# Kernel tuning notes

Measured on AMD Instinct MI355X. Metric: run time of the kernel, lower is better.

## Reference

```python
import jax, jax.numpy as jnp
import numpy as np

EMBED_DIM = 128
B, SQ, SKV = 16, 2048, 2048


def setup_inputs() -> dict:
    key = jax.random.key(0)
    ks = jax.random.split(key, 8)
    d = EMBED_DIM
    scale = 1.0 / np.sqrt(d)
    return {
        "x": jax.random.normal(ks[0], (B, SQ, d), dtype=jnp.float32),
        "y": jax.random.normal(ks[1], (B, SKV, d), dtype=jnp.float32),
        "Wq": jax.random.normal(ks[2], (d, d), dtype=jnp.float32) * scale,
        "bq": jax.random.normal(ks[3], (d,), dtype=jnp.float32) * 0.02,
        "Wk": jax.random.normal(ks[4], (d, d), dtype=jnp.float32) * scale,
        "bk": jax.random.normal(ks[5], (d,), dtype=jnp.float32) * 0.02,
        "Wv": jax.random.normal(ks[6], (d, d), dtype=jnp.float32) * scale,
        "bv": jax.random.normal(ks[7], (d,), dtype=jnp.float32) * 0.02,
    }


def reference(x, y, Wq, bq, Wk, bk, Wv, bv):
    # Linear projections (torch Linear: x @ W.T + b; here W stored as [in,out])
    q = x @ Wq + bq            # [B, SQ, d]
    k = y @ Wk + bk            # [B, SKV, d]
    v = y @ Wv + bv            # [B, SKV, d]
    # Source scales by q.size(-1)**0.5 = sqrt(embed_dim)
    inv_scale = 1.0 / jnp.sqrt(jnp.asarray(q.shape[-1], q.dtype))
    scores = jnp.einsum("bqd,bkd->bqk", q, k) * inv_scale  # [B, SQ, SKV]
    attn = jax.nn.softmax(scores, axis=-1)
    return jnp.einsum("bqk,bkd->bqd", attn, v)
```

## Files before the change

kernel.cpp:

```cpp
#include <hip/hip_runtime.h>
#include <hip/hip_bf16.h>

typedef unsigned short ushort_t;
typedef __attribute__((ext_vector_type(8))) short short8;
typedef __attribute__((ext_vector_type(4))) float f32x4;
typedef __attribute__((ext_vector_type(16))) float f32x16;

#define MFMA16(a, b, c) __builtin_amdgcn_mfma_f32_16x16x32_bf16((a), (b), (c), 0, 0, 0)
#define MFMA32(a, b, c) __builtin_amdgcn_mfma_f32_32x32x16_bf16((a), (b), (c), 0, 0, 0)

__device__ __forceinline__ ushort_t f2bf(float f) {
    return __builtin_bit_cast(ushort_t, __float2bfloat16(f));
}

#define CVTPK(lo, hi) ({ unsigned int r_; \
    asm("v_cvt_pk_bf16_f32 %0, %1, %2" : "=v"(r_) : "v"(lo), "v"(hi)); r_; })

__device__ __forceinline__ void gl_lds16(const void* g, void* l) {
    __builtin_amdgcn_global_load_lds((const __attribute__((address_space(1))) void*)g,
                                     (__attribute__((address_space(3))) void*)l, 16, 0, 0);
}

__global__ __launch_bounds__(256) void proj3(
    const float* __restrict__ x, const float* __restrict__ y,
    const float* __restrict__ Wq, const float* __restrict__ bq,
    const float* __restrict__ Wk, const float* __restrict__ bk,
    const float* __restrict__ Wv, const float* __restrict__ bv,
    ushort_t* __restrict__ Qd, ushort_t* __restrict__ Kd, ushort_t* __restrict__ VTd,
    float qscale)
{
    __shared__ __align__(16) char smem[65536];

    const int t = threadIdx.x;
    const int mat = blockIdx.x >> 9;
    const int pb  = blockIdx.x & 511;
    const float* src = (mat == 0) ? x : y;
    const float* W   = (mat == 0) ? Wq : (mat == 1) ? Wk : Wv;
    const float* bb  = (mat == 0) ? bq : (mat == 1) ? bk : bv;
    const float  sc  = (mat == 0) ? qscale : 1.0f;

    const int w  = t >> 6;
    const int l  = t & 63;
    const int lg = l >> 4;
    const int ln = l & 15;
    const int acol = lg * 8;

    {
        const char* srcb = (const char*)(src + (size_t)(pb * 64) * 128);
        #pragma unroll
        for (int i = 0; i < 8; ++i) {
            int off = i * 4096 + w * 1024 + l * 16;
            int soff = off ^ (((off >> 9) & 7) << 4);
            gl_lds16(srcb + soff, smem + i * 4096 + w * 1024);
        }
    }

    char* wt = smem + 32768;
    #pragma unroll
    for (int i = 0; i < 16; ++i) {
        int idx = t + i * 256;
        int k  = idx >> 5;
        int c0 = (idx & 31) * 4;
        f32x4 v = ((const f32x4*)W)[idx];
        #pragma unroll
        for (int j = 0; j < 4; ++j) {
            int c = c0 + j;
            int byte = (c * 256 + k * 2) ^ ((c & 7) << 4);
            *(ushort_t*)(wt + byte) = f2bf(v[j]);
        }
    }
    __syncthreads();

    short8 afrag[4];
    {
        const int row = w * 16 + ln;
        const int sw = (row & 7) << 4;
        #pragma unroll
        for (int kc = 0; kc < 4; ++kc) {
            int off0 = row * 512 + lg * 32 + kc * 128;
            f32x4 a0 = *(const f32x4*)(smem + (off0 ^ sw));
            f32x4 a1 = *(const f32x4*)(smem + ((off0 + 16) ^ sw));
            short8 a;
            #pragma unroll
            for (int j = 0; j < 4; ++j) { a[j] = (short)f2bf(a0[j]); a[4 + j] = (short)f2bf(a1[j]); }
            afrag[kc] = a;
        }
    }
    __syncthreads();

    if (mat < 2) {
        ushort_t* tile = (ushort_t*)smem;
        #pragma unroll
        for (int ct = 0; ct < 8; ++ct) {
            f32x4 acc = {0.f, 0.f, 0.f, 0.f};
            const int c = ct * 16 + ln;
            #pragma unroll
            for (int kc = 0; kc < 4; ++kc) {
                int byte = (c * 256 + (kc * 32 + acol) * 2) ^ ((c & 7) << 4);
                short8 bfr = *(const short8*)(wt + byte);
                acc = MFMA16(afrag[kc], bfr, acc);
            }
            float bvv = bb[c];
            #pragma unroll
            for (int reg = 0; reg < 4; ++reg)
                tile[(w * 16 + lg * 4 + reg) * 144 + c] = f2bf((acc[reg] + bvv) * sc);
        }
        __syncthreads();
        const int row = t >> 2, ch = t & 3;
        ushort_t* dst1 = (mat == 0 ? Qd : Kd) + (size_t)(pb * 64 + row) * 128 + ch * 32;
        #pragma unroll
        for (int j = 0; j < 4; ++j)
            *(short8*)(dst1 + j * 8) = *(const short8*)&tile[row * 144 + ch * 32 + j * 8];
    } else {
        ushort_t* vt = (ushort_t*)smem;
        #pragma unroll
        for (int ct = 0; ct < 8; ++ct) {
            f32x4 acc = {0.f, 0.f, 0.f, 0.f};
            const int c = ct * 16 + ln;
            #pragma unroll
            for (int kc = 0; kc < 4; ++kc) {
                int byte = (c * 256 + (kc * 32 + acol) * 2) ^ ((c & 7) << 4);
                short8 bfr = *(const short8*)(wt + byte);
                acc = MFMA16(afrag[kc], bfr, acc);
            }
            float bvv = bb[c];
            #pragma unroll
            for (int reg = 0; reg < 4; ++reg) {
                int rloc = w * 16 + lg * 4 + reg;
                int byte = (c * 128 + rloc * 2) ^ ((c & 7) << 4);
                *(ushort_t*)((char*)vt + byte) = f2bf(acc[reg] + bvv);
            }
        }
        __syncthreads();
        const int r0b = pb * 64;
        const int b   = r0b >> 11;
        const int kv0 = r0b & 2047;
        const int c    = t >> 1;
        const int half = t & 1;
        ushort_t* dst = VTd + (size_t)b * 128 * 2048 + (size_t)c * 2048 + kv0 + half * 32;
        #pragma unroll
        for (int j = 0; j < 4; ++j) {
            int byte = (c * 128 + (half * 32 + j * 8) * 2) ^ ((c & 7) << 4);
            *(short8*)(dst + j * 8) = *(const short8*)((const char*)vt + byte);
        }
    }
}

#define KVBLK 64
#define NT (2048 / KVBLK)
__global__ __launch_bounds__(256) void attn_kernel(
    const ushort_t* __restrict__ Q, const ushort_t* __restrict__ K,
    const ushort_t* __restrict__ VT, float* __restrict__ out)
{
    __shared__ __align__(16) char smem_[81920];

    const int t = threadIdx.x;
    const int bid = (int)blockIdx.x;
    const int wg = (bid & 7) * 64 + (bid >> 3);
    const int b  = wg >> 5;
    const int q0blk = (wg & 31) * 64;

    const char* Kb  = (const char*)(K  + (size_t)b * 2048 * 128);
    const char* VTb = (const char*)(VT + (size_t)b * 128 * 2048);
    const ushort_t* Qb = Q + (size_t)b * 2048 * 128;

    const int w   = t >> 6;
    const int qg  = w >> 1;
    const int kvh = w & 1;
    const int l  = t & 63;
    const int lq = l & 31;
    const int h  = l >> 5;
    const int q0 = q0blk + qg * 32;

    short8 qfrag[8];
    {
        const ushort_t* qp = Qb + (size_t)(q0 + lq) * 128 + h * 8;
        #pragma unroll
        for (int kc = 0; kc < 8; ++kc)
            qfrag[kc] = *(const short8*)(qp + kc * 16);
    }

    f32x16 o[4];
    #pragma unroll
    for (int db = 0; db < 4; ++db)
        #pragma unroll
        for (int i = 0; i < 16; ++i) o[db][i] = 0.f;
    f32x16 ls;
    #pragma unroll
    for (int i = 0; i < 16; ++i) ls[i] = 0.f;

    auto stageK = [&](char* kd, int kt) {
        const char* kb = Kb + (size_t)kt * KVBLK * 256;
        #pragma unroll
        for (int i = 0; i < 4; ++i) {
            int base = w * 4096 + i * 1024;
            int p = base + l * 16;
            int pl = p ^ (((p >> 8) & 15) << 4);
            gl_lds16(kb + pl, kd + base);
        }
    };
    auto stageV = [&](char* vd, int kt) {
        const int kv2 = kt * KVBLK * 2;
        #pragma unroll
        for (int i = 0; i < 4; ++i) {
            int base = w * 4096 + i * 1024;
            int p = base + l * 16;
            int pl = p ^ (((p >> 8) & 15) << 4);
            int dv = ((pl >> 8) << 1) | ((pl >> 7) & 1);
            gl_lds16(VTb + (size_t)dv * 4096 + kv2 + (pl & 127), vd + base);
        }
    };

    char* p0 = smem_;
    char* p1 = smem_ + 16384;
    char* p2 = smem_ + 32768;
    char* p3 = smem_ + 49152;
    char* p4 = smem_ + 65536;

    stageK(p0, 0);
    stageV(p1, 0);
    stageK(p2, 1);
    stageV(p3, 1);

    for (int kt = 0; kt < NT; ++kt) {
        const int kt2 = (kt + 2 < NT) ? kt + 2 : 0;

        asm volatile("s_waitcnt vmcnt(12)" ::: "memory");
        __builtin_amdgcn_s_barrier();
        stageK(p4, kt2);

        f32x16 s;
        #pragma unroll
        for (int i = 0; i < 16; ++i) s[i] = 0.f;
        const int krow = kvh * 32 + lq;
        const int ksw = (krow & 15) << 4;
        __builtin_amdgcn_s_setprio(1);
        #pragma unroll
        for (int kc = 0; kc < 8; ++kc) {
            int col = (h * 16 + kc * 32) ^ ksw;
            short8 kf = *(const short8*)(p0 + krow * 256 + col);
            s = MFMA32(kf, qfrag[kc], s);
        }
        __builtin_amdgcn_s_setprio(0);

        #pragma unroll
        for (int i = 0; i < 16; ++i) s[i] = __builtin_exp2f(s[i]);
        #pragma unroll
        for (int i = 0; i < 16; ++i) ls[i] += s[i];

        short8 pf[2];
        {
            auto pack2 = [&](int a, short8& outf) {
                unsigned u0 = CVTPK(s[a * 8 + 0], s[a * 8 + 1]);
                unsigned u1 = CVTPK(s[a * 8 + 2], s[a * 8 + 3]);
                unsigned u2 = CVTPK(s[a * 8 + 4], s[a * 8 + 5]);
                unsigned u3 = CVTPK(s[a * 8 + 6], s[a * 8 + 7]);
                asm("v_permlane32_swap_b32 %0, %1" : "+v"(u0), "+v"(u2));
                asm("v_permlane32_swap_b32 %0, %1" : "+v"(u1), "+v"(u3));
                union { unsigned wds[4]; short8 s8; } f;
                f.wds[0] = u0; f.wds[1] = u1; f.wds[2] = u2; f.wds[3] = u3;
                outf = f.s8;
            };
            pack2(0, pf[0]);
            pack2(1, pf[1]);
        }

        asm volatile("s_waitcnt vmcnt(12)" ::: "memory");
        __builtin_amdgcn_s_barrier();
        stageV(p0, kt2);

        __builtin_amdgcn_s_setprio(1);
        #pragma unroll
        for (int db = 0; db < 4; ++db) {
            int d = db * 32 + lq;
            int vrow = d >> 1;
            int vsw = (vrow & 15) << 4;
            #pragma unroll
            for (int ks = 0; ks < 2; ++ks) {
                int colb = ((d & 1) << 7) | (kvh * 64 + ks * 32 + h * 16);
                short8 vf = *(const short8*)(p1 + vrow * 256 + (colb ^ vsw));
                o[db] = MFMA32(vf, pf[ks], o[db]);
            }
        }
        __builtin_amdgcn_s_setprio(0);

        char* n0 = p2; char* n1 = p3; char* n2 = p4; char* n3 = p0; char* n4 = p1;
        p0 = n0; p1 = n1; p2 = n2; p3 = n3; p4 = n4;
    }

    asm volatile("s_waitcnt vmcnt(0)" ::: "memory");

    float lsum;
    {
        float a8[8];
        #pragma unroll
        for (int i = 0; i < 8; ++i) a8[i] = ls[i] + ls[i + 8];
        #pragma unroll
        for (int i = 0; i < 4; ++i) a8[i] += a8[i + 4];
        lsum = (a8[0] + a8[1]) + (a8[2] + a8[3]);
    }
    lsum += __shfl_xor(lsum, 32);

    __syncthreads();
    float* mrg = (float*)smem_;
    const int mo = qg * 4224 + lq * 132;
    const int mlb = 8448;

    if (kvh == 1) {
        #pragma unroll
        for (int db = 0; db < 4; ++db) {
            #pragma unroll
            for (int rq = 0; rq < 4; ++rq) {
                f32x4 v4;
                #pragma unroll
                for (int j = 0; j < 4; ++j) v4[j] = o[db][rq * 4 + j];
                *(f32x4*)&mrg[mo + db * 32 + rq * 8 + 4 * h] = v4;
            }
        }
        if (h == 0) mrg[mlb + qg * 64 + lq] = lsum;
    }
    __syncthreads();
    if (kvh == 0) {
        float inv = 1.0f / (lsum + mrg[mlb + qg * 64 + lq]);
        float* ob = out + (size_t)b * 2048 * 128 + (size_t)(q0 + lq) * 128;
        #pragma unroll
        for (int db = 0; db < 4; ++db) {
            #pragma unroll
            for (int rq = 0; rq < 4; ++rq) {
                f32x4 p4v = *(const f32x4*)&mrg[mo + db * 32 + rq * 8 + 4 * h];
                f32x4 st;
                #pragma unroll
                for (int j = 0; j < 4; ++j)
                    st[j] = (o[db][rq * 4 + j] + p4v[j]) * inv;
                *(f32x4*)(ob + db * 32 + rq * 8 + 4 * h) = st;
            }
        }
    }
}

extern "C" void kernel_launch(void* const* d_in, const int* in_sizes, int n_in,
                              void* d_out, int out_size, void* d_ws, size_t ws_size,
                              hipStream_t stream) {
    (void)in_sizes; (void)n_in; (void)out_size; (void)ws_size;
    const float* x  = (const float*)d_in[0];
    const float* y  = (const float*)d_in[1];
    const float* Wq = (const float*)d_in[2];
    const float* bq = (const float*)d_in[3];
    const float* Wk = (const float*)d_in[4];
    const float* bk = (const float*)d_in[5];
    const float* Wv = (const float*)d_in[6];
    const float* bv = (const float*)d_in[7];
    float* out = (float*)d_out;

    ushort_t* qws  = (ushort_t*)d_ws;
    ushort_t* kws  = qws + (size_t)32768 * 128;
    ushort_t* vtws = kws + (size_t)32768 * 128;

    const float qscale = (float)(1.4426950408889634 / 11.313708498984761);

    proj3<<<1536, 256, 0, stream>>>(x, y, Wq, bq, Wk, bk, Wv, bv, qws, kws, vtws, qscale);
    attn_kernel<<<512, 256, 0, stream>>>(qws, kws, vtws, out);
}
```

Before: 94.21 us.

## Prefetch K fragments into registers and split QK accumulation into two chains

```diff
diff --git a/kernel.cpp b/kernel.cpp
--- a/kernel.cpp
+++ b/kernel.cpp
@@ -211,40 +211,53 @@
         }
     };
 
-    char* p0 = smem_;
-    char* p1 = smem_ + 16384;
-    char* p2 = smem_ + 32768;
-    char* p3 = smem_ + 49152;
-    char* p4 = smem_ + 65536;
-
-    stageK(p0, 0);
-    stageV(p1, 0);
-    stageK(p2, 1);
-    stageV(p3, 1);
+    const int krow = kvh * 32 + lq;
+    const int ksw = (krow & 15) << 4;
+    short8 kf[8];
+    auto prefK = [&](const char* kb) {
+        #pragma unroll
+        for (int kc = 0; kc < 8; ++kc) {
+            int col = (h * 16 + kc * 32) ^ ksw;
+            kf[kc] = *(const short8*)(kb + krow * 256 + col);
+        }
+    };
+
+    char* sA = smem_ + 16384;
+    char* sB = smem_ + 32768;
+    char* sC = smem_ + 49152;
+    char* sD = smem_;
+    char* sE = smem_ + 65536;
+
+    stageK(sD, 0);
+    stageV(sA, 0);
+    stageK(sB, 1);
+    stageV(sC, 1);
+    asm volatile("s_waitcnt vmcnt(12)" ::: "memory");
+    __builtin_amdgcn_s_barrier();
+    prefK(sD);
 
     for (int kt = 0; kt < NT; ++kt) {
         const int kt2 = (kt + 2 < NT) ? kt + 2 : 0;
 
-        asm volatile("s_waitcnt vmcnt(12)" ::: "memory");
+        asm volatile("s_waitcnt lgkmcnt(0)" ::: "memory");
         __builtin_amdgcn_s_barrier();
-        stageK(p4, kt2);
+        stageK(sD, kt2);
+        stageV(sE, kt2);
+
+        f32x16 sa, sb;
+        #pragma unroll
+        for (int i = 0; i < 16; ++i) { sa[i] = 0.f; sb[i] = 0.f; }
+        __builtin_amdgcn_s_setprio(1);
+        #pragma unroll
+        for (int kc = 0; kc < 4; ++kc) {
+            sa = MFMA32(kf[kc], qfrag[kc], sa);
+            sb = MFMA32(kf[4 + kc], qfrag[4 + kc], sb);
+        }
+        __builtin_amdgcn_s_setprio(0);
 
         f32x16 s;
         #pragma unroll
-        for (int i = 0; i < 16; ++i) s[i] = 0.f;
-        const int krow = kvh * 32 + lq;
-        const int ksw = (krow & 15) << 4;
-        __builtin_amdgcn_s_setprio(1);
-        #pragma unroll
-        for (int kc = 0; kc < 8; ++kc) {
-            int col = (h * 16 + kc * 32) ^ ksw;
-            short8 kf = *(const short8*)(p0 + krow * 256 + col);
-            s = MFMA32(kf, qfrag[kc], s);
-        }
-        __builtin_amdgcn_s_setprio(0);
-
-        #pragma unroll
-        for (int i = 0; i < 16; ++i) s[i] = __builtin_exp2f(s[i]);
+        for (int i = 0; i < 16; ++i) s[i] = __builtin_exp2f(sa[i] + sb[i]);
         #pragma unroll
         for (int i = 0; i < 16; ++i) ls[i] += s[i];
 
@@ -265,9 +278,8 @@
             pack2(1, pf[1]);
         }
 
-        asm volatile("s_waitcnt vmcnt(12)" ::: "memory");
+        asm volatile("s_waitcnt vmcnt(8)" ::: "memory");
         __builtin_amdgcn_s_barrier();
-        stageV(p0, kt2);
 
         __builtin_amdgcn_s_setprio(1);
         #pragma unroll
@@ -278,14 +290,15 @@
             #pragma unroll
             for (int ks = 0; ks < 2; ++ks) {
                 int colb = ((d & 1) << 7) | (kvh * 64 + ks * 32 + h * 16);
-                short8 vf = *(const short8*)(p1 + vrow * 256 + (colb ^ vsw));
+                short8 vf = *(const short8*)(sA + vrow * 256 + (colb ^ vsw));
                 o[db] = MFMA32(vf, pf[ks], o[db]);
             }
         }
         __builtin_amdgcn_s_setprio(0);
-
-        char* n0 = p2; char* n1 = p3; char* n2 = p4; char* n3 = p0; char* n4 = p1;
-        p0 = n0; p1 = n1; p2 = n2; p3 = n3; p4 = n4;
+        prefK(sB);
+
+        char* nA = sC; char* nB = sD; char* nC = sE; char* nD = sB; char* nE = sA;
+        sA = nA; sB = nB; sC = nC; sD = nD; sE = nE;
     }
 
     asm volatile("s_waitcnt vmcnt(0)" ::: "memory");
```

Measured after the change: 100.3 us. 6.5% more time.
